# Kernel tuning notes

Hardware: AMD Instinct MI355X
Metric: run time of the kernel (lower is better)

Reference implementation:

```python
import jax, jax.numpy as jnp
import numpy as np

N_HEADS = 12


def setup_inputs() -> dict:
    key = jax.random.key(0)
    ks = jax.random.split(key, 5)
    B, T, D = 4, 2048, 768
    std = 1.0 / np.sqrt(D)
    return {
        "x": jax.random.normal(ks[0], (B, T, D), jnp.float32),
        "W_qkv": jax.random.normal(ks[1], (3 * D, D), jnp.float32) * std,
        "b_qkv": jax.random.normal(ks[2], (3 * D,), jnp.float32) * 0.02,
        "W_proj": jax.random.normal(ks[3], (D, D), jnp.float32) * std,
        "b_proj": jax.random.normal(ks[4], (D,), jnp.float32) * 0.02,
    }


def reference(x, W_qkv, b_qkv, W_proj, b_proj):
    # x: [B, T, D]; intended 3D path of the module (dropout = eval-mode identity)
    B, T, D = x.shape
    H = N_HEADS
    Dh = D // H
    scale = Dh ** -0.5
    qkv = x @ W_qkv.T + b_qkv                       # [B, T, 3D]
    qkv = qkv.reshape(B, T, 3, H, Dh)
    q = jnp.transpose(qkv[:, :, 0], (0, 2, 1, 3))    # [B, H, T, Dh]
    k = jnp.transpose(qkv[:, :, 1], (0, 2, 1, 3))
    v = jnp.transpose(qkv[:, :, 2], (0, 2, 1, 3))
    attn = jnp.einsum("bhqd,bhkd->bhqk", q, k) * scale  # [B, H, T, T]
    scores = jax.nn.softmax(attn, axis=-1)
    out = jnp.einsum("bhqk,bhkd->bhqd", scores, v)       # [B, H, T, Dh]
    out = jnp.transpose(out, (0, 2, 1, 3)).reshape(B, T, D)
    return out @ W_proj.T + b_proj
```

## Files before the change

kernel.cpp:

```cpp
#include <hip/hip_runtime.h>
#include <hip/hip_bf16.h>
#include <stdint.h>

typedef __bf16 bf16;
typedef __bf16 bf16x8 __attribute__((ext_vector_type(8)));
typedef __bf16 bf16x4 __attribute__((ext_vector_type(4)));
typedef short  s16x4  __attribute__((ext_vector_type(4)));
typedef short  s16x8  __attribute__((ext_vector_type(8)));
typedef float  f32x4  __attribute__((ext_vector_type(4)));

#define N_B 4
#define N_T 2048
#define N_D 768
#define N_H 12
#define N_DH 64
#define M_TOT (N_B * N_T)

__device__ __forceinline__ void async_copy16(const bf16* g, bf16* l) {
    __builtin_amdgcn_global_load_lds(
        (const __attribute__((address_space(1))) unsigned int*)g,
        (__attribute__((address_space(3))) unsigned int*)l,
        16, 0, 0);
}

__launch_bounds__(256)
__global__ void f2bf3(const float* __restrict__ a, bf16* __restrict__ oa, int na,
                      const float* __restrict__ b, bf16* __restrict__ ob, int nb,
                      const float* __restrict__ c, bf16* __restrict__ oc) {
    int i = (blockIdx.x * 256 + threadIdx.x) * 4;
    const float* src; bf16* dst;
    if (i < na)            { src = a; dst = oa; }
    else if (i < na + nb)  { src = b; dst = ob; i -= na; }
    else                   { src = c; dst = oc; i -= na + nb; }
    const float4 v = *(const float4*)(src + i);
    dst[i]     = (bf16)v.x;
    dst[i + 1] = (bf16)v.y;
    dst[i + 2] = (bf16)v.z;
    dst[i + 3] = (bf16)v.w;
}

#define GEMM_CORE(A_PTR, B_PTR, KDIM)                                          \
    __shared__ bf16 lsA[128 * 32];                                             \
    __shared__ bf16 lsB[128 * 32];                                             \
    const int m0 = blockIdx.x * 128;                                           \
    const int n0 = blockIdx.y * 128;                                           \
    const int t  = threadIdx.x;                                                \
    const int w  = t >> 6, l = t & 63;                                         \
    const int wm = w & 1, wn = w >> 1;                                         \
    const int lr = l & 15, lq = l >> 4;                                        \
    f32x4 acc[4][4] = {};                                                      \
    const bf16* Ab = (A_PTR) + (size_t)(m0 + (t >> 2)) * (KDIM) + (t & 3) * 8; \
    const bf16* Bb = (B_PTR) + (size_t)(n0 + (t >> 2)) * (KDIM) + (t & 3) * 8; \
    bf16* lA = lsA + t * 8;                                                    \
    bf16* lB = lsB + t * 8;                                                    \
    for (int k0 = 0; k0 < (KDIM); k0 += 32) {                                  \
        __syncthreads();                                                       \
        async_copy16(Ab + k0, lA);                                             \
        async_copy16(Ab + (size_t)64 * (KDIM) + k0, lA + 2048);                \
        async_copy16(Bb + k0, lB);                                             \
        async_copy16(Bb + (size_t)64 * (KDIM) + k0, lB + 2048);                \
        __syncthreads();                                                       \
        bf16x8 af[4], bfr[4];                                                  \
        for (int i = 0; i < 4; i++) {                                          \
            af[i]  = *(const bf16x8*)(lsA + (wm * 64 + i * 16 + lr) * 32 + lq * 8); \
            bfr[i] = *(const bf16x8*)(lsB + (wn * 64 + i * 16 + lr) * 32 + lq * 8); \
        }                                                                      \
        for (int i = 0; i < 4; i++)                                            \
            for (int j = 0; j < 4; j++)                                        \
                acc[i][j] = __builtin_amdgcn_mfma_f32_16x16x32_bf16(           \
                    af[i], bfr[j], acc[i][j], 0, 0, 0);                        \
    }

__launch_bounds__(256)
__global__ void gemm_qkv(const bf16* __restrict__ X, const bf16* __restrict__ W,
                         const float* __restrict__ bias,
                         bf16* __restrict__ Q, bf16* __restrict__ K,
                         bf16* __restrict__ Vt) {
    GEMM_CORE(X, W, 768)
    for (int i = 0; i < 4; i++) {
        const int rowb = m0 + wm * 64 + i * 16 + lq * 4;
        const int b_ = rowb >> 11, tt = rowb & 2047;
        for (int j = 0; j < 4; j++) {
            const int col   = n0 + wn * 64 + j * 16 + lr;
            const int which = col / 768;
            const int rem   = col - which * 768;
            const int h     = rem >> 6, d = rem & 63;
            const float bv  = bias[col];
            if (which == 2) {
                const int tile = tt >> 6, kl = tt & 63;
                const int kc = kl >> 4, r = kl & 15;
                const int idx = ((r >> 2) << 4) + (kc << 2);
                bf16x4 v4;
                for (int r2 = 0; r2 < 4; r2++) v4[r2] = (bf16)(acc[i][j][r2] + bv);
                *(bf16x4*)(Vt + ((size_t)((b_ * N_H + h) * 64 + d)) * 2048
                           + tile * 64 + idx) = v4;
            } else {
                bf16* dst = (which == 0) ? Q : K;
                const float sc = (which == 0) ? 0.18033688f : 1.0f;
                for (int r2 = 0; r2 < 4; r2++)
                    dst[(size_t)(((b_ * N_H + h) << 11) + tt + r2) * 64 + d] =
                        (bf16)((acc[i][j][r2] + bv) * sc);
            }
        }
    }
}

__launch_bounds__(256)
__global__ void gemm_proj(const bf16* __restrict__ O, const bf16* __restrict__ W,
                          const float* __restrict__ bias, float* __restrict__ out) {
    GEMM_CORE(O, W, 768)
    for (int i = 0; i < 4; i++) {
        const int rowb = m0 + wm * 64 + i * 16 + lq * 4;
        for (int j = 0; j < 4; j++) {
            const int col  = n0 + wn * 64 + j * 16 + lr;
            const float bv = bias[col];
            for (int r = 0; r < 4; r++)
                out[(size_t)(rowb + r) * 768 + col] = acc[i][j][r] + bv;
        }
    }
}

__launch_bounds__(256, 3)
__global__ void attn(const bf16* __restrict__ Q, const bf16* __restrict__ K,
                     const bf16* __restrict__ Vt, bf16* __restrict__ O) {
    __shared__ bf16 lsK[2][64 * 64];
    __shared__ bf16 lsV[2][64 * 64];
    const int bid = blockIdx.x;
    const int xcd = bid & 7, slot = bid >> 3;
    const int bh  = xcd + 8 * (slot >> 4);
    const int qt  = slot & 15;
    const int t = threadIdx.x, w = t >> 6, l = t & 63;
    const int lr = l & 15, lq = l >> 4;
    const bf16* Qh  = Q  + (size_t)bh * N_T * 64;
    const bf16* Kh  = K  + (size_t)bh * N_T * 64;
    const bf16* Vth = Vt + (size_t)bh * 64 * N_T;
    const int q0 = qt * 128 + w * 32;

    bf16x8 qf[2][2];
    #pragma unroll
    for (int qg = 0; qg < 2; qg++)
        #pragma unroll
        for (int ks = 0; ks < 2; ks++)
            qf[qg][ks] = *(const bf16x8*)(Qh + (size_t)(q0 + qg * 16 + lr) * 64
                                          + ks * 32 + lq * 8);

    f32x4 oacc[2][4] = {};
    f32x4 lacc[2]    = {};
    const s16x4 ones = {0x3F80, 0x3F80, 0x3F80, 0x3F80};

    #pragma unroll
    for (int j = 0; j < 2; j++) {
        const int u   = t + j * 256;
        const int row = u >> 3;
        const int scn = (u & 7) ^ (row & 7);
        async_copy16(Kh  + (size_t)row * 64 + scn * 8,   lsK[0] + u * 8);
        async_copy16(Vth + (size_t)row * 2048 + scn * 8, lsV[0] + u * 8);
    }

    for (int kt = 0; kt < 32; kt++) {
        const int cur = kt & 1;
        __syncthreads();

        if (kt < 31) {
            #pragma unroll
            for (int j = 0; j < 2; j++) {
                const int u   = t + j * 256;
                const int row = u >> 3;
                const int scn = (u & 7) ^ (row & 7);
                async_copy16(Kh + (size_t)((kt + 1) * 64 + row) * 64 + scn * 8,
                             lsK[cur ^ 1] + u * 8);
                async_copy16(Vth + (size_t)row * 2048 + (kt + 1) * 64 + scn * 8,
                             lsV[cur ^ 1] + u * 8);
            }
        }

        bf16x8 kf[2][4];
        #pragma unroll
        for (int ks = 0; ks < 2; ks++)
            #pragma unroll
            for (int ki = 0; ki < 4; ki++) {
                const int row = ki * 16 + lr;
                kf[ks][ki] = *(const bf16x8*)(lsK[cur] + row * 64
                                              + ((ks * 4 + lq) ^ (lr & 7)) * 8);
            }

        s16x4 pbf[2][4];
        #pragma unroll
        for (int qg = 0; qg < 2; qg++) {
            f32x4 sacc[4] = {};
            #pragma unroll
            for (int ks = 0; ks < 2; ks++)
                #pragma unroll
                for (int ki = 0; ki < 4; ki++)
                    sacc[ki] = __builtin_amdgcn_mfma_f32_16x16x32_bf16(
                        kf[ks][ki], qf[qg][ks], sacc[ki], 0, 0, 0);
            #pragma unroll
            for (int ki = 0; ki < 4; ki++) {
                bf16x4 pb;
                #pragma unroll
                for (int r = 0; r < 4; r++)
                    pb[r] = (bf16)exp2f(sacc[ki][r]);
                pbf[qg][ki] = __builtin_bit_cast(s16x4, pb);
            }
        }

        #pragma unroll
        for (int c = 0; c < 2; c++)
            #pragma unroll
            for (int dj = 0; dj < 4; dj++) {
                const int row  = dj * 16 + lr;
                const int unit = (2 * lq + c) ^ (lr & 7);
                s16x8 vv = *(const s16x8*)(lsV[cur] + row * 64 + unit * 8);
                s16x4 vlo = __builtin_shufflevector(vv, vv, 0, 1, 2, 3);
                s16x4 vhi = __builtin_shufflevector(vv, vv, 4, 5, 6, 7);
                #pragma unroll
                for (int qg = 0; qg < 2; qg++) {
                    oacc[qg][dj] = __builtin_amdgcn_mfma_f32_16x16x16bf16_1k(
                        vlo, pbf[qg][2 * c], oacc[qg][dj], 0, 0, 0);
                    oacc[qg][dj] = __builtin_amdgcn_mfma_f32_16x16x16bf16_1k(
                        vhi, pbf[qg][2 * c + 1], oacc[qg][dj], 0, 0, 0);
                }
            }
        #pragma unroll
        for (int qg = 0; qg < 2; qg++)
            #pragma unroll
            for (int kc = 0; kc < 4; kc++)
                lacc[qg] = __builtin_amdgcn_mfma_f32_16x16x16bf16_1k(
                    ones, pbf[qg][kc], lacc[qg], 0, 0, 0);
    }

    const int b = bh / N_H, h = bh - b * N_H;
    #pragma unroll
    for (int qg = 0; qg < 2; qg++) {
        const float inv_l = 1.0f / lacc[qg][0];
        const int tok = q0 + qg * 16 + lr;
        bf16* Ob = O + ((size_t)b * N_T + tok) * N_D + h * 64;
        #pragma unroll
        for (int dj = 0; dj < 4; dj++) {
            bf16x4 o4;
            #pragma unroll
            for (int r = 0; r < 4; r++) o4[r] = (bf16)(oacc[qg][dj][r] * inv_l);
            *(bf16x4*)(Ob + dj * 16 + lq * 4) = o4;
        }
    }
}

extern "C" void kernel_launch(void* const* d_in, const int* in_sizes, int n_in,
                              void* d_out, int out_size, void* d_ws, size_t ws_size,
                              hipStream_t stream) {
    const float* x      = (const float*)d_in[0];
    const float* W_qkv  = (const float*)d_in[1];
    const float* b_qkv  = (const float*)d_in[2];
    const float* W_proj = (const float*)d_in[3];
    const float* b_proj = (const float*)d_in[4];
    float* out = (float*)d_out;

    char* ws = (char*)d_ws;
    const size_t n_x  = (size_t)M_TOT * N_D;
    const size_t n_wq = (size_t)3 * N_D * N_D;
    const size_t n_wp = (size_t)N_D * N_D;
    const size_t sz_qkv = (size_t)N_B * N_H * N_T * N_DH * sizeof(bf16);

    bf16* xb  = (bf16*)(ws);                 ws += n_x * sizeof(bf16);
    bf16* Wqb = (bf16*)(ws);                 ws += n_wq * sizeof(bf16);
    bf16* Wpb = (bf16*)(ws);                 ws += n_wp * sizeof(bf16);
    bf16* Qb  = (bf16*)(ws);                 ws += sz_qkv;
    bf16* Kb  = (bf16*)(ws);                 ws += sz_qkv;
    bf16* Vtb = (bf16*)(ws);                 ws += sz_qkv;
    bf16* Ob  = (bf16*)(ws);

    dim3 blk(256);
    f2bf3<<<dim3((int)((n_x + n_wq + n_wp) / 1024)), blk, 0, stream>>>(
        x, xb, (int)n_x, W_qkv, Wqb, (int)n_wq, W_proj, Wpb);

    gemm_qkv<<<dim3(M_TOT / 128, 2304 / 128), blk, 0, stream>>>(xb, Wqb, b_qkv, Qb, Kb, Vtb);
    attn<<<dim3(768), dim3(256), 0, stream>>>(Qb, Kb, Vtb, Ob);
    gemm_proj<<<dim3(M_TOT / 128, 768 / 128), blk, 0, stream>>>(Ob, Wpb, b_proj, out);
}
```

Measured before the change: 230.8 us.

## Use 16x16x32 MFMA for PV and row-sum with matching V layout

Switches the P·V and row-sum accumulation from 16x16x16 bf16 MFMAs to 16x16x32 MFMAs, halving the number of matrix instructions per tile. The P fragments are packed as 8-wide vectors from two score tiles, and the V-transpose layout written by the QKV GEMM epilogue is permuted so that each lane's 8-element LDS read lines up with the new k ordering. It also raises wave priority around the MFMA blocks with s_setprio to favour matrix issue over the exp work. The risk is that the permuted layout must exactly match the fragment ordering, or results are silently wrong.

New measurement: 222.1 us. 1.04x faster.

```diff
diff --git a/kernel.cpp b/kernel.cpp
--- a/kernel.cpp
+++ b/kernel.cpp
@@ -88,8 +88,8 @@
             const float bv  = bias[col];
             if (which == 2) {
                 const int tile = tt >> 6, kl = tt & 63;
-                const int kc = kl >> 4, r = kl & 15;
-                const int idx = ((r >> 2) << 4) + (kc << 2);
+                const int ki = kl >> 4, lqv = (kl >> 2) & 3;
+                const int idx = 32 * (ki & 1) + 8 * lqv + 4 * (ki >> 1);
                 bf16x4 v4;
                 for (int r2 = 0; r2 < 4; r2++) v4[r2] = (bf16)(acc[i][j][r2] + bv);
                 *(bf16x4*)(Vt + ((size_t)((b_ * N_H + h) * 64 + d)) * 2048
@@ -146,7 +146,8 @@
 
     f32x4 oacc[2][4] = {};
     f32x4 lacc[2]    = {};
-    const s16x4 ones = {0x3F80, 0x3F80, 0x3F80, 0x3F80};
+    const bf16x8 ones8 = {(bf16)1.f, (bf16)1.f, (bf16)1.f, (bf16)1.f,
+                          (bf16)1.f, (bf16)1.f, (bf16)1.f, (bf16)1.f};
 
     #pragma unroll
     for (int j = 0; j < 2; j++) {
@@ -184,49 +185,50 @@
                                               + ((ks * 4 + lq) ^ (lr & 7)) * 8);
             }
 
-        s16x4 pbf[2][4];
+        bf16x8 pbf[2][2];
         #pragma unroll
         for (int qg = 0; qg < 2; qg++) {
             f32x4 sacc[4] = {};
+            __builtin_amdgcn_s_setprio(1);
             #pragma unroll
             for (int ks = 0; ks < 2; ks++)
                 #pragma unroll
                 for (int ki = 0; ki < 4; ki++)
                     sacc[ki] = __builtin_amdgcn_mfma_f32_16x16x32_bf16(
                         kf[ks][ki], qf[qg][ks], sacc[ki], 0, 0, 0);
-            #pragma unroll
-            for (int ki = 0; ki < 4; ki++) {
-                bf16x4 pb;
+            __builtin_amdgcn_s_setprio(0);
+            #pragma unroll
+            for (int ks = 0; ks < 2; ks++) {
+                bf16x8 pb;
                 #pragma unroll
-                for (int r = 0; r < 4; r++)
-                    pb[r] = (bf16)exp2f(sacc[ki][r]);
-                pbf[qg][ki] = __builtin_bit_cast(s16x4, pb);
-            }
-        }
-
-        #pragma unroll
-        for (int c = 0; c < 2; c++)
+                for (int r = 0; r < 4; r++) {
+                    pb[r]     = (bf16)exp2f(sacc[ks][r]);
+                    pb[4 + r] = (bf16)exp2f(sacc[ks + 2][r]);
+                }
+                pbf[qg][ks] = pb;
+            }
+        }
+
+        __builtin_amdgcn_s_setprio(1);
+        #pragma unroll
+        for (int ks = 0; ks < 2; ks++)
             #pragma unroll
             for (int dj = 0; dj < 4; dj++) {
                 const int row  = dj * 16 + lr;
-                const int unit = (2 * lq + c) ^ (lr & 7);
-                s16x8 vv = *(const s16x8*)(lsV[cur] + row * 64 + unit * 8);
-                s16x4 vlo = __builtin_shufflevector(vv, vv, 0, 1, 2, 3);
-                s16x4 vhi = __builtin_shufflevector(vv, vv, 4, 5, 6, 7);
+                const int unit = (4 * ks + lq) ^ (lr & 7);
+                bf16x8 vf = *(const bf16x8*)(lsV[cur] + row * 64 + unit * 8);
                 #pragma unroll
-                for (int qg = 0; qg < 2; qg++) {
-                    oacc[qg][dj] = __builtin_amdgcn_mfma_f32_16x16x16bf16_1k(
-                        vlo, pbf[qg][2 * c], oacc[qg][dj], 0, 0, 0);
-                    oacc[qg][dj] = __builtin_amdgcn_mfma_f32_16x16x16bf16_1k(
-                        vhi, pbf[qg][2 * c + 1], oacc[qg][dj], 0, 0, 0);
-                }
+                for (int qg = 0; qg < 2; qg++)
+                    oacc[qg][dj] = __builtin_amdgcn_mfma_f32_16x16x32_bf16(
+                        vf, pbf[qg][ks], oacc[qg][dj], 0, 0, 0);
             }
         #pragma unroll
         for (int qg = 0; qg < 2; qg++)
             #pragma unroll
-            for (int kc = 0; kc < 4; kc++)
-                lacc[qg] = __builtin_amdgcn_mfma_f32_16x16x16bf16_1k(
-                    ones, pbf[qg][kc], lacc[qg], 0, 0, 0);
+            for (int ks = 0; ks < 2; ks++)
+                lacc[qg] = __builtin_amdgcn_mfma_f32_16x16x32_bf16(
+                    ones8, pbf[qg][ks], lacc[qg], 0, 0, 0);
+        __builtin_amdgcn_s_setprio(0);
     }
 
     const int b = bh / N_H, h = bh - b * N_H;
```
